# Kernel tuning notes

Hardware: AMD Instinct MI355X
Metric: run time of the kernel (lower is better)

## Reference

```python
import jax, jax.numpy as jnp
import numpy as np

N_FFT = 256
HOP = 64            # fft_stride
WIN_LEN = 1024      # window_length (samples)
STRIDE = 256        # MPF window stride (samples)
FS = 2000.0
BANDS = [(0.0, 25.0), (25.0, 50.0), (50.0, 100.0), (100.0, 200.0), (200.0, 400.0), (400.0, 1000.0)]


def setup_inputs() -> dict:
    key = jax.random.key(0)
    x = jax.random.normal(key, (8, 32, 16000), dtype=jnp.float32)
    return {"inputs": x}


def _mpf_forward(inputs):
    # --- channelwise STFT (center=False, onesided, hann periodic=False) ---
    window = jnp.asarray(np.hanning(N_FFT), dtype=inputs.dtype)  # matches torch.hann_window(periodic=False)
    wnorm = jnp.linalg.norm(window)
    B, C, T = inputs.shape
    n_frames = 1 + (T - N_FFT) // HOP
    fidx = np.arange(n_frames)[:, None] * HOP + np.arange(N_FFT)[None, :]
    frames = inputs[..., fidx]                       # (B, C, n_frames, n_fft)
    spec = jnp.fft.rfft(frames * window, axis=-1) / wnorm  # (B, C, n_frames, F)
    spec = jnp.swapaxes(spec, -1, -2)                # (B, C, F, n_frames)

    # --- sliding window over STFT frames ---
    size = WIN_LEN // HOP   # 16
    step = STRIDE // HOP    # 4
    n_win = (n_frames - size) // step + 1
    widx = np.arange(n_win)[:, None] * step + np.arange(size)[None, :]
    win = spec[..., widx]                            # (B, C, F, n_win, size)
    x = jnp.transpose(win, (0, 3, 2, 1, 4))          # (B, n_win, F, C, size)

    # --- cross-spectral density: X X^H / size, then |.|^2 ---
    csd = jnp.einsum('btfcw,btfdw->btfcd', x, jnp.conj(x)) / size
    csd = csd.real ** 2 + csd.imag ** 2              # (B, n_win, F, C, C) real

    # --- average FFT bins into frequency bands ---
    freqs = np.fft.rfftfreq(N_FFT, d=1.0 / FS)
    masks_np = np.stack([(freqs > lo) & (freqs <= hi) for lo, hi in BANDS]).astype(np.float32)
    masks = jnp.asarray(masks_np, dtype=csd.dtype)   # (n_bands, F)
    banded = jnp.einsum('btfcd,kf->btkcd', csd, masks) / masks.sum(axis=1)[None, None, :, None, None]

    # --- SPD matrix log via eigh, eigvals floored at 100*eps ---
    eigvals, eigvecs = jnp.linalg.eigh(banded)
    floor = 100.0 * jnp.finfo(banded.dtype).eps
    log_vals = jnp.log(jnp.maximum(eigvals, floor))
    out = jnp.einsum('...ij,...j,...kj->...ik', eigvecs, log_vals, eigvecs)

    # (batch, time, bands, c1, c2) -> (batch, bands, c1, c2, time)
    return jnp.transpose(out, (0, 2, 3, 4, 1))


def reference(inputs) -> jnp.ndarray:
    return _mpf_forward(inputs)
```

## Files before the change

### kernel.cpp

```cpp
#include <hip/hip_runtime.h>
#include <cstddef>

#define NFRM 247
#define NBIN 128
#define NC   32
#define NWIN 58
#define NMAT (8 * NWIN * 6)

__global__ __launch_bounds__(128) void k_stft(const float* __restrict__ x,
                                              float2* __restrict__ spec) {
  const int gid = blockIdx.x;
  const int fr  = gid % NFRM;
  const int bc  = gid / NFRM;
  const int tid = threadIdx.x;

  __shared__ float  xw[256];
  __shared__ float2 Y[256];

  const float* xp = x + ((size_t)bc * 16000 + (size_t)fr * 64);

  #pragma unroll
  for (int k = 0; k < 2; ++k) {
    const int t = tid + k * 128;
    const float wv = 0.5f - 0.5f * __cosf((float)t * 0.024639942f);
    xw[t] = xp[t] * wv * 0.10226200f;
  }
  __syncthreads();

  #pragma unroll
  for (int k = 0; k < 2; ++k) {
    const int e = tid + k * 128;
    const int f0 = e >> 4, t0 = e & 15;
    float sA, cA;
    __sincosf((float)f0 * 0.39269908f, &sA, &cA);
    float wr = 1.f, wi = 0.f, re = 0.f, im = 0.f;
    #pragma unroll
    for (int t1 = 0; t1 < 16; ++t1) {
      const float v = xw[(t1 << 4) + t0];
      re = fmaf(v, wr, re);
      im = fmaf(v, wi, im);
      const float nwr = fmaf(wi, sA, wr * cA);
      const float nwi = fmaf(-wr, sA, wi * cA);
      wr = nwr; wi = nwi;
    }
    Y[e] = make_float2(re, im);
  }
  __syncthreads();

  const int f = tid + 1;
  const int f0 = f & 15;
  float sB, cB;
  __sincosf((float)f * 0.024543693f, &sB, &cB);
  float wr = 1.f, wi = 0.f, re = 0.f, im = 0.f;
  #pragma unroll
  for (int t0 = 0; t0 < 16; ++t0) {
    const float2 yv = Y[(f0 << 4) + t0];
    re += yv.x * wr - yv.y * wi;
    im += yv.x * wi + yv.y * wr;
    const float nwr = fmaf(wi, sB, wr * cB);
    const float nwi = fmaf(-wr, sB, wi * cB);
    wr = nwr; wi = nwi;
  }
  const int b = bc >> 5, c = bc & 31;
  spec[(((size_t)b * NFRM + fr) * NBIN + (f - 1)) * NC + c] = make_float2(re, im);
}

__global__ __launch_bounds__(256) void k_csd(const float2* __restrict__ spec,
                                             float* __restrict__ part, int P) {
  const int bt  = blockIdx.x;
  const int p   = blockIdx.y;
  const int b   = bt / NWIN, t = bt % NWIN;
  const int tid = threadIdx.x;
  const int wv  = tid >> 6;
  const int lane = tid & 63;
  const int i0 = (lane >> 3) * 4;
  const int j0 = (lane & 7) * 4;

  __shared__ __align__(16) char smemraw[32768];
  float2 (*rng)[2][512] = reinterpret_cast<float2 (*)[2][512]>(smemraw);
  float* red = reinterpret_cast<float*>(smemraw);

  float bacc[6][16];
  #pragma unroll
  for (int k = 0; k < 6; ++k)
    #pragma unroll
    for (int e = 0; e < 16; ++e) bacc[k][e] = 0.f;

  const float2* sb = spec + (size_t)b * NFRM * NBIN * NC;
  const int itn = 32 / P;

  #define STG_LOAD(itl, dst)                                                     \
    {                                                                            \
      const int f_ = 1 + wv + 4 * (itn * p + (itl));                             \
      const float2* fp_ = sb + (size_t)(f_ - 1) * NC;                            \
      _Pragma("unroll")                                                          \
      for (int r = 0; r < 8; ++r) {                                              \
        const int e_ = lane + r * 64;                                            \
        dst[r] = fp_[(size_t)(t * 4 + (e_ >> 5)) * (NBIN * NC) + (e_ & 31)];     \
      }                                                                          \
    }

  {
    float2 stg[8];
    STG_LOAD(0, stg)
    float2* Xs = rng[wv][0];
    #pragma unroll
    for (int r = 0; r < 8; ++r) Xs[lane + r * 64] = stg[r];
  }

  for (int itl = 0; itl < itn; ++itl) {
    float2 stg2[8];
    if (itl + 1 < itn) STG_LOAD(itl + 1, stg2)

    const int f = 1 + wv + 4 * (itn * p + itl);
    const float2* Xs = rng[wv][itl & 1];

    float accRe[16], accIm[16];
    #pragma unroll
    for (int e = 0; e < 16; ++e) { accRe[e] = 0.f; accIm[e] = 0.f; }

    #pragma unroll
    for (int s = 0; s < 16; ++s) {
      float2 xi[4], xj[4];
      #pragma unroll
      for (int a = 0; a < 4; ++a) {
        xi[a] = Xs[s * 32 + i0 + a];
        xj[a] = Xs[s * 32 + j0 + a];
      }
      #pragma unroll
      for (int a = 0; a < 4; ++a)
        #pragma unroll
        for (int d = 0; d < 4; ++d) {
          const int e = a * 4 + d;
          accRe[e] = fmaf(xi[a].x, xj[d].x, fmaf(xi[a].y, xj[d].y, accRe[e]));
          accIm[e] = fmaf(xi[a].y, xj[d].x, fmaf(-xi[a].x, xj[d].y, accIm[e]));
        }
    }

    #define ACCB(K) { _Pragma("unroll") \
      for (int e = 0; e < 16; ++e) { float rr = accRe[e], ii = accIm[e]; \
        bacc[K][e] = fmaf(rr, rr, fmaf(ii, ii, bacc[K][e])); } }
    if      (f <= 3)  ACCB(0)
    else if (f <= 6)  ACCB(1)
    else if (f <= 12) ACCB(2)
    else if (f <= 25) ACCB(3)
    else if (f <= 51) ACCB(4)
    else              ACCB(5)
    #undef ACCB

    if (itl + 1 < itn) {
      float2* Xn = rng[wv][(itl + 1) & 1];
      #pragma unroll
      for (int r = 0; r < 8; ++r) Xn[lane + r * 64] = stg2[r];
    }
  }
  #undef STG_LOAD

  __syncthreads();

  for (int w2 = 0; w2 < 4; ++w2) {
    if (wv == w2) {
      #pragma unroll
      for (int k = 0; k < 6; ++k)
        #pragma unroll
        for (int a = 0; a < 4; ++a)
          #pragma unroll
          for (int d = 0; d < 4; ++d) {
            const int idx = k * 1024 + (i0 + a) * 32 + (j0 + d);
            const float v = bacc[k][a * 4 + d];
            if (w2 == 0) red[idx] = v; else red[idx] += v;
          }
    }
    __syncthreads();
  }

  float* op = part + ((size_t)p * (8 * NWIN) + bt) * 6144;
  for (int u = tid; u < 6144; u += 256) {
    const int k = u >> 10;
    float scl;
    if      (k <= 1) scl = 1.f / 768.f;
    else if (k == 2) scl = 1.f / 1536.f;
    else if (k == 3) scl = 1.f / 3328.f;
    else if (k == 4) scl = 1.f / 6656.f;
    else             scl = 1.f / 19712.f;
    op[u] = red[u] * scl;
  }
}

__global__ __launch_bounds__(64) void k_eig(const float* __restrict__ part,
                                            float* __restrict__ eigTmp, int P) {
  const int blk  = blockIdx.x;
  const int lane = threadIdx.x;
  const int h    = lane >> 5;
  const int c    = lane & 31;

  __shared__ float sA[32][36];
  __shared__ float sSc[32];

  for (int u = lane; u < 1024; u += 64) {
    const size_t base = (size_t)blk * 1024 + u;
    float s = 0.f;
    for (int p = 0; p < P; ++p) s += part[(size_t)p * ((size_t)NMAT * 1024) + base];
    sA[u >> 5][u & 31] = s;
  }
  __syncthreads();

  float g[16];
  #pragma unroll
  for (int i = 0; i < 16; ++i) g[i] = sA[16 * h + i][c];

  float n;
  {
    float p0 = 0.f, p1 = 0.f, p2 = 0.f, p3 = 0.f;
    #pragma unroll
    for (int e = 0; e < 16; e += 4) {
      p0 = fmaf(g[e + 0], g[e + 0], p0);
      p1 = fmaf(g[e + 1], g[e + 1], p1);
      p2 = fmaf(g[e + 2], g[e + 2], p2);
      p3 = fmaf(g[e + 3], g[e + 3], p3);
    }
    const float pp = (p0 + p1) + (p2 + p3);
    const float op = __shfl_xor(pp, 32);
    n = h ? (op + pp) : (pp + op);
  }

  const float EPS2 = 1e-7f;
  #pragma unroll 1
  for (int sweep = 0; sweep < 10; ++sweep) {
    int anybad = 0;
    #pragma unroll 1
    for (int m = 1; m < 32; ++m) {
      const int pidx = (lane ^ m) << 2;
      float tmp[16];
      #pragma unroll
      for (int e = 0; e < 16; ++e)
        tmp[e] = __int_as_float(__builtin_amdgcn_ds_bpermute(pidx, __float_as_int(g[e])));
      const float np = __int_as_float(__builtin_amdgcn_ds_bpermute(pidx, __float_as_int(n)));

      float d0 = 0.f, d1 = 0.f, d2 = 0.f, d3 = 0.f;
      #pragma unroll
      for (int e = 0; e < 16; e += 4) {
        d0 = fmaf(g[e + 0], tmp[e + 0], d0);
        d1 = fmaf(g[e + 1], tmp[e + 1], d1);
        d2 = fmaf(g[e + 2], tmp[e + 2], d2);
        d3 = fmaf(g[e + 3], tmp[e + 3], d3);
      }
      const float pp = (d0 + d1) + (d2 + d3);
      const float op = __shfl_xor(pp, 32);
      const float bpq = h ? (op + pp) : (pp + op);

      const int bad = (bpq * bpq > EPS2 * n * np);
      anybad |= bad;
      if (bad) {
        const float tau = (np - n) * 0.5f * __builtin_amdgcn_rcpf(bpq);
        float tf = __builtin_amdgcn_rcpf(fabsf(tau) + __builtin_amdgcn_sqrtf(fmaf(tau, tau, 1.f)));
        if (tau < 0.f) tf = -tf;
        const float cr = __builtin_amdgcn_rsqf(fmaf(tf, tf, 1.f));
        const float sg = -tf * cr;
        n = fmaf(-tf, bpq, n);
        #pragma unroll
        for (int e = 0; e < 16; ++e) g[e] = fmaf(sg, tmp[e], cr * g[e]);
      }
    }
    if (!__any(anybad)) break;
  }

  float nx;
  {
    float p0 = 0.f, p1 = 0.f, p2 = 0.f, p3 = 0.f;
    #pragma unroll
    for (int e = 0; e < 16; e += 4) {
      p0 = fmaf(g[e + 0], g[e + 0], p0);
      p1 = fmaf(g[e + 1], g[e + 1], p1);
      p2 = fmaf(g[e + 2], g[e + 2], p2);
      p3 = fmaf(g[e + 3], g[e + 3], p3);
    }
    const float pp = (p0 + p1) + (p2 + p3);
    const float op = __shfl_xor(pp, 32);
    nx = h ? (op + pp) : (pp + op);
  }
  const float lv = 0.5f * __logf(fmaxf(nx, 1.4210855e-10f));
  const float sc = (nx > 1e-32f) ? (lv * __builtin_amdgcn_rcpf(nx)) : 0.f;

  __syncthreads();
  #pragma unroll
  for (int i = 0; i < 16; ++i) sA[c][16 * h + i] = g[i];
  if (h == 0) sSc[c] = sc;
  __syncthreads();

  float a[32];
  #pragma unroll
  for (int e = 0; e < 32; ++e) a[e] = sSc[e] * sA[e][c];

  float* ob = eigTmp + ((size_t)blk * 1024 + c * 32 + 16 * h);
  #pragma unroll
  for (int q = 0; q < 4; ++q) {
    float4 acc = make_float4(0.f, 0.f, 0.f, 0.f);
    #pragma unroll
    for (int e = 0; e < 32; ++e) {
      const float4 gv = *(const float4*)&sA[e][16 * h + 4 * q];
      acc.x = fmaf(a[e], gv.x, acc.x);
      acc.y = fmaf(a[e], gv.y, acc.y);
      acc.z = fmaf(a[e], gv.z, acc.z);
      acc.w = fmaf(a[e], gv.w, acc.w);
    }
    *(float4*)(ob + 4 * q) = acc;
  }
}

__global__ __launch_bounds__(256) void k_tr(const float* __restrict__ eigTmp,
                                            float* __restrict__ out) {
  const int bk    = blockIdx.x >> 3;
  const int chunk = blockIdx.x & 7;
  const int b = bk / 6, k = bk % 6;
  const int ij0 = chunk * 128;
  const int tid = threadIdx.x;

  __shared__ float tile[128 * 59];

  for (int u = tid; u < 128 * NWIN; u += 256) {
    const int t = u >> 7, ijl = u & 127;
    tile[ijl * 59 + t] = eigTmp[((size_t)(b * NWIN + t) * 6 + k) * 1024 + ij0 + ijl];
  }
  __syncthreads();

  float* ob = out + ((size_t)bk * 1024 + ij0) * NWIN;
  for (int u = tid; u < 128 * NWIN; u += 256) {
    ob[u] = tile[(u / NWIN) * 59 + (u % NWIN)];
  }
}

extern "C" void kernel_launch(void* const* d_in, const int* in_sizes, int n_in,
                              void* d_out, int out_size, void* d_ws, size_t ws_size,
                              hipStream_t stream) {
  const float* x = (const float*)d_in[0];
  float* outp = (float*)d_out;

  const size_t SPEC_B = (size_t)8 * NFRM * NBIN * NC * sizeof(float2);
  const size_t BAND_B = (size_t)NMAT * 1024 * sizeof(float);

  float2* spec   = (float2*)d_ws;
  float*  part   = (float*)((char*)d_ws + SPEC_B);
  float*  eigTmp = (float*)d_ws;

  int P = 1;
  if (ws_size >= SPEC_B + 2 * BAND_B) P = 2;

  k_stft<<<dim3(8 * 32 * NFRM), dim3(128), 0, stream>>>(x, spec);
  k_csd <<<dim3(8 * NWIN, P),   dim3(256), 0, stream>>>(spec, part, P);
  k_eig <<<dim3(NMAT),          dim3(64),  0, stream>>>(part, eigTmp, P);
  k_tr  <<<dim3(48 * 8),        dim3(256), 0, stream>>>(eigTmp, outp);
}
```

Before: 455.1 us.

## Split CSD frequency accumulation into two specialized phase kernels

Replaces the single CSD kernel, which split frequencies into P halves, with two templated kernels covering bins 1-48 (five bands) and 49-128 (two bands). Each kernel keeps only the band accumulators it needs, which cuts register pressure and lets the launch bounds request higher occupancy. It also reorders block indices so consecutive blocks are spread across batches. The eig kernel now reads the two partial buffers and sums only band 4, which spans both phases. In exchange there is one extra kernel launch, and the two phases do unequal amounts of work.

```diff
diff --git a/kernel.cpp b/kernel.cpp
--- a/kernel.cpp
+++ b/kernel.cpp
@@ -6,6 +6,7 @@
 #define NC   32
 #define NWIN 58
 #define NMAT (8 * NWIN * 6)
+#define NBT  (8 * NWIN)
 
 __global__ __launch_bounds__(128) void k_stft(const float* __restrict__ x,
                                               float2* __restrict__ spec) {
@@ -65,10 +66,14 @@
   spec[(((size_t)b * NFRM + fr) * NBIN + (f - 1)) * NC + c] = make_float2(re, im);
 }
 
-__global__ __launch_bounds__(256) void k_csd(const float2* __restrict__ spec,
-                                             float* __restrict__ part, int P) {
-  const int bt  = blockIdx.x;
-  const int p   = blockIdx.y;
+template<int PHASE>
+__global__ __launch_bounds__(256, PHASE == 0 ? 3 : 4)
+void k_csd(const float2* __restrict__ spec, float* __restrict__ part) {
+  constexpr int FSTART = PHASE == 0 ? 1 : 49;
+  constexpr int ITN    = PHASE == 0 ? 12 : 20;
+  constexpr int NB     = PHASE == 0 ? 5 : 2;
+
+  const int bt  = (blockIdx.x & 7) * 58 + (blockIdx.x >> 3);
   const int b   = bt / NWIN, t = bt % NWIN;
   const int tid = threadIdx.x;
   const int wv  = tid >> 6;
@@ -80,18 +85,17 @@
   float2 (*rng)[2][512] = reinterpret_cast<float2 (*)[2][512]>(smemraw);
   float* red = reinterpret_cast<float*>(smemraw);
 
-  float bacc[6][16];
-  #pragma unroll
-  for (int k = 0; k < 6; ++k)
+  float bacc[NB][16];
+  #pragma unroll
+  for (int k = 0; k < NB; ++k)
     #pragma unroll
     for (int e = 0; e < 16; ++e) bacc[k][e] = 0.f;
 
   const float2* sb = spec + (size_t)b * NFRM * NBIN * NC;
-  const int itn = 32 / P;
 
   #define STG_LOAD(itl, dst)                                                     \
     {                                                                            \
-      const int f_ = 1 + wv + 4 * (itn * p + (itl));                             \
+      const int f_ = FSTART + wv + 4 * (itl);                                    \
       const float2* fp_ = sb + (size_t)(f_ - 1) * NC;                            \
       _Pragma("unroll")                                                          \
       for (int r = 0; r < 8; ++r) {                                              \
@@ -108,11 +112,11 @@
     for (int r = 0; r < 8; ++r) Xs[lane + r * 64] = stg[r];
   }
 
-  for (int itl = 0; itl < itn; ++itl) {
+  for (int itl = 0; itl < ITN; ++itl) {
     float2 stg2[8];
-    if (itl + 1 < itn) STG_LOAD(itl + 1, stg2)
-
-    const int f = 1 + wv + 4 * (itn * p + itl);
+    if (itl + 1 < ITN) STG_LOAD(itl + 1, stg2)
+
+    const int f = FSTART + wv + 4 * itl;
     const float2* Xs = rng[wv][itl & 1];
 
     float accRe[16], accIm[16];
@@ -140,15 +144,19 @@
     #define ACCB(K) { _Pragma("unroll") \
       for (int e = 0; e < 16; ++e) { float rr = accRe[e], ii = accIm[e]; \
         bacc[K][e] = fmaf(rr, rr, fmaf(ii, ii, bacc[K][e])); } }
-    if      (f <= 3)  ACCB(0)
-    else if (f <= 6)  ACCB(1)
-    else if (f <= 12) ACCB(2)
-    else if (f <= 25) ACCB(3)
-    else if (f <= 51) ACCB(4)
-    else              ACCB(5)
+    if constexpr (PHASE == 0) {
+      if      (f <= 3)  ACCB(0)
+      else if (f <= 6)  ACCB(1)
+      else if (f <= 12) ACCB(2)
+      else if (f <= 25) ACCB(3)
+      else              ACCB(4)
+    } else {
+      if      (f <= 51) ACCB(0)
+      else              ACCB(1)
+    }
     #undef ACCB
 
-    if (itl + 1 < itn) {
+    if (itl + 1 < ITN) {
       float2* Xn = rng[wv][(itl + 1) & 1];
       #pragma unroll
       for (int r = 0; r < 8; ++r) Xn[lane + r * 64] = stg2[r];
@@ -161,7 +169,7 @@
   for (int w2 = 0; w2 < 4; ++w2) {
     if (wv == w2) {
       #pragma unroll
-      for (int k = 0; k < 6; ++k)
+      for (int k = 0; k < NB; ++k)
         #pragma unroll
         for (int a = 0; a < 4; ++a)
           #pragma unroll
@@ -174,33 +182,42 @@
     __syncthreads();
   }
 
-  float* op = part + ((size_t)p * (8 * NWIN) + bt) * 6144;
-  for (int u = tid; u < 6144; u += 256) {
+  float* op = part + (size_t)bt * (NB * 1024);
+  for (int u = tid; u < NB * 1024; u += 256) {
     const int k = u >> 10;
     float scl;
-    if      (k <= 1) scl = 1.f / 768.f;
-    else if (k == 2) scl = 1.f / 1536.f;
-    else if (k == 3) scl = 1.f / 3328.f;
-    else if (k == 4) scl = 1.f / 6656.f;
-    else             scl = 1.f / 19712.f;
+    if constexpr (PHASE == 0) {
+      if      (k <= 1) scl = 1.f / 768.f;
+      else if (k == 2) scl = 1.f / 1536.f;
+      else if (k == 3) scl = 1.f / 3328.f;
+      else             scl = 1.f / 6656.f;
+    } else {
+      scl = (k == 0) ? (1.f / 6656.f)
+                     : (1.f / 19712.f);
+    }
     op[u] = red[u] * scl;
   }
 }
 
-__global__ __launch_bounds__(64) void k_eig(const float* __restrict__ part,
-                                            float* __restrict__ eigTmp, int P) {
+__global__ __launch_bounds__(64) void k_eig(const float* __restrict__ partA,
+                                            const float* __restrict__ partB,
+                                            float* __restrict__ eigTmp) {
   const int blk  = blockIdx.x;
   const int lane = threadIdx.x;
   const int h    = lane >> 5;
   const int c    = lane & 31;
 
+  const int kq = blk % 6;
+  const int bt = blk / 6;
+
   __shared__ float sA[32][36];
   __shared__ float sSc[32];
 
   for (int u = lane; u < 1024; u += 64) {
-    const size_t base = (size_t)blk * 1024 + u;
-    float s = 0.f;
-    for (int p = 0; p < P; ++p) s += part[(size_t)p * ((size_t)NMAT * 1024) + base];
+    float s;
+    if (kq <= 3)      s = partA[(size_t)bt * 5120 + kq * 1024 + u];
+    else if (kq == 4) s = partA[(size_t)bt * 5120 + 4096 + u] + partB[(size_t)bt * 2048 + u];
+    else              s = partB[(size_t)bt * 2048 + 1024 + u];
     sA[u >> 5][u & 31] = s;
   }
   __syncthreads();
@@ -336,18 +353,17 @@
   const float* x = (const float*)d_in[0];
   float* outp = (float*)d_out;
 
-  const size_t SPEC_B = (size_t)8 * NFRM * NBIN * NC * sizeof(float2);
-  const size_t BAND_B = (size_t)NMAT * 1024 * sizeof(float);
+  const size_t SPEC_B  = (size_t)8 * NFRM * NBIN * NC * sizeof(float2);
+  const size_t PARTA_B = (size_t)NBT * 5120 * sizeof(float);
 
   float2* spec   = (float2*)d_ws;
-  float*  part   = (float*)((char*)d_ws + SPEC_B);
+  float*  partA  = (float*)((char*)d_ws + SPEC_B);
+  float*  partB  = (float*)((char*)d_ws + SPEC_B + PARTA_B);
   float*  eigTmp = (float*)d_ws;
 
-  int P = 1;
-  if (ws_size >= SPEC_B + 2 * BAND_B) P = 2;
-
-  k_stft<<<dim3(8 * 32 * NFRM), dim3(128), 0, stream>>>(x, spec);
-  k_csd <<<dim3(8 * NWIN, P),   dim3(256), 0, stream>>>(spec, part, P);
-  k_eig <<<dim3(NMAT),          dim3(64),  0, stream>>>(part, eigTmp, P);
-  k_tr  <<<dim3(48 * 8),        dim3(256), 0, stream>>>(eigTmp, outp);
-}
+  k_stft   <<<dim3(8 * 32 * NFRM), dim3(128), 0, stream>>>(x, spec);
+  k_csd<0> <<<dim3(NBT),           dim3(256), 0, stream>>>(spec, partA);
+  k_csd<1> <<<dim3(NBT),           dim3(256), 0, stream>>>(spec, partB);
+  k_eig    <<<dim3(NMAT),          dim3(64),  0, stream>>>(partA, partB, eigTmp);
+  k_tr     <<<dim3(48 * 8),        dim3(256), 0, stream>>>(eigTmp, outp);
+}
```

Measured after the change: 492.7 us. 1.08x slower.

## Assign contiguous frequency ranges per wave and drop shared-memory band reduction

Applied to the files above, without the earlier changes.

Each wave now processes 16 consecutive frequency bins instead of interleaved bins, so it keeps one running band accumulator and writes a partial matrix to a per-slot buffer whenever it crosses a band boundary. This removes the 6x16 register accumulator array, the serialized four-step shared-memory reduction with syncthreads, and the 24KB reduction pass. The eigen kernel then sums a variable number of slot partials per band. It also always launches the split-by-2 grid and assumes the workspace holds 13 slots of partials without checking ws_size.

```diff
diff --git a/kernel.cpp b/kernel.cpp
--- a/kernel.cpp
+++ b/kernel.cpp
@@ -6,6 +6,7 @@
 #define NC   32
 #define NWIN 58
 #define NMAT (8 * NWIN * 6)
+#define NBT  (8 * NWIN)
 
 __global__ __launch_bounds__(128) void k_stft(const float* __restrict__ x,
                                               float2* __restrict__ spec) {
@@ -66,7 +67,7 @@
 }
 
 __global__ __launch_bounds__(256) void k_csd(const float2* __restrict__ spec,
-                                             float* __restrict__ part, int P) {
+                                             float* __restrict__ part) {
   const int bt  = blockIdx.x;
   const int p   = blockIdx.y;
   const int b   = bt / NWIN, t = bt % NWIN;
@@ -76,22 +77,42 @@
   const int i0 = (lane >> 3) * 4;
   const int j0 = (lane & 7) * 4;
 
-  __shared__ __align__(16) char smemraw[32768];
-  float2 (*rng)[2][512] = reinterpret_cast<float2 (*)[2][512]>(smemraw);
-  float* red = reinterpret_cast<float*>(smemraw);
-
-  float bacc[6][16];
-  #pragma unroll
-  for (int k = 0; k < 6; ++k)
-    #pragma unroll
-    for (int e = 0; e < 16; ++e) bacc[k][e] = 0.f;
+  __shared__ __align__(16) float2 rng[4][2][512];
+
+  float bacc[16];
+  #pragma unroll
+  for (int e = 0; e < 16; ++e) bacc[e] = 0.f;
 
   const float2* sb = spec + (size_t)b * NFRM * NBIN * NC;
-  const int itn = 32 / P;
+  const int fbase = 1 + 64 * p + 16 * wv;
+  int slot = p ? (9 + wv) : (wv == 0 ? 0 : wv == 1 ? 4 : wv == 2 ? 6 : 7);
+
+  #define BANDOF(f) ((f) <= 3 ? 0 : (f) <= 6 ? 1 : (f) <= 12 ? 2 : (f) <= 25 ? 3 : (f) <= 51 ? 4 : 5)
+  int curband = BANDOF(fbase);
+
+  #define FLUSH()                                                                \
+    {                                                                            \
+      float scl_;                                                                \
+      switch (curband) {                                                         \
+        case 0: case 1: scl_ = 1.f / 768.f;   break;                             \
+        case 2:         scl_ = 1.f / 1536.f;  break;                             \
+        case 3:         scl_ = 1.f / 3328.f;  break;                             \
+        case 4:         scl_ = 1.f / 6656.f;  break;                             \
+        default:        scl_ = 1.f / 19712.f; break;                             \
+      }                                                                          \
+      float* op_ = part + ((size_t)slot * NBT + bt) * 1024;                      \
+      _Pragma("unroll")                                                          \
+      for (int a = 0; a < 4; ++a)                                                \
+        *(float4*)(op_ + (i0 + a) * 32 + j0) =                                   \
+          make_float4(bacc[a * 4 + 0] * scl_, bacc[a * 4 + 1] * scl_,            \
+                      bacc[a * 4 + 2] * scl_, bacc[a * 4 + 3] * scl_);           \
+      _Pragma("unroll")                                                          \
+      for (int e = 0; e < 16; ++e) bacc[e] = 0.f;                                \
+    }
 
   #define STG_LOAD(itl, dst)                                                     \
     {                                                                            \
-      const int f_ = 1 + wv + 4 * (itn * p + (itl));                             \
+      const int f_ = fbase + (itl);                                              \
       const float2* fp_ = sb + (size_t)(f_ - 1) * NC;                            \
       _Pragma("unroll")                                                          \
       for (int r = 0; r < 8; ++r) {                                              \
@@ -103,16 +124,22 @@
   {
     float2 stg[8];
     STG_LOAD(0, stg)
-    float2* Xs = rng[wv][0];
-    #pragma unroll
-    for (int r = 0; r < 8; ++r) Xs[lane + r * 64] = stg[r];
-  }
-
-  for (int itl = 0; itl < itn; ++itl) {
+    #pragma unroll
+    for (int r = 0; r < 8; ++r) rng[wv][0][lane + r * 64] = stg[r];
+  }
+
+  #pragma unroll 1
+  for (int itl = 0; itl < 16; ++itl) {
     float2 stg2[8];
-    if (itl + 1 < itn) STG_LOAD(itl + 1, stg2)
-
-    const int f = 1 + wv + 4 * (itn * p + itl);
+    if (itl + 1 < 16) STG_LOAD(itl + 1, stg2)
+
+    const int f = fbase + itl;
+    if (f == 4 || f == 7 || f == 13 || f == 26 || f == 52) {
+      FLUSH()
+      ++slot;
+      curband = BANDOF(f);
+    }
+
     const float2* Xs = rng[wv][itl & 1];
 
     float accRe[16], accIm[16];
@@ -137,70 +164,40 @@
         }
     }
 
-    #define ACCB(K) { _Pragma("unroll") \
-      for (int e = 0; e < 16; ++e) { float rr = accRe[e], ii = accIm[e]; \
-        bacc[K][e] = fmaf(rr, rr, fmaf(ii, ii, bacc[K][e])); } }
-    if      (f <= 3)  ACCB(0)
-    else if (f <= 6)  ACCB(1)
-    else if (f <= 12) ACCB(2)
-    else if (f <= 25) ACCB(3)
-    else if (f <= 51) ACCB(4)
-    else              ACCB(5)
-    #undef ACCB
-
-    if (itl + 1 < itn) {
-      float2* Xn = rng[wv][(itl + 1) & 1];
-      #pragma unroll
-      for (int r = 0; r < 8; ++r) Xn[lane + r * 64] = stg2[r];
-    }
-  }
+    #pragma unroll
+    for (int e = 0; e < 16; ++e)
+      bacc[e] = fmaf(accRe[e], accRe[e], fmaf(accIm[e], accIm[e], bacc[e]));
+
+    if (itl + 1 < 16) {
+      #pragma unroll
+      for (int r = 0; r < 8; ++r) rng[wv][(itl + 1) & 1][lane + r * 64] = stg2[r];
+    }
+  }
+  FLUSH()
   #undef STG_LOAD
-
-  __syncthreads();
-
-  for (int w2 = 0; w2 < 4; ++w2) {
-    if (wv == w2) {
-      #pragma unroll
-      for (int k = 0; k < 6; ++k)
-        #pragma unroll
-        for (int a = 0; a < 4; ++a)
-          #pragma unroll
-          for (int d = 0; d < 4; ++d) {
-            const int idx = k * 1024 + (i0 + a) * 32 + (j0 + d);
-            const float v = bacc[k][a * 4 + d];
-            if (w2 == 0) red[idx] = v; else red[idx] += v;
-          }
-    }
-    __syncthreads();
-  }
-
-  float* op = part + ((size_t)p * (8 * NWIN) + bt) * 6144;
-  for (int u = tid; u < 6144; u += 256) {
-    const int k = u >> 10;
-    float scl;
-    if      (k <= 1) scl = 1.f / 768.f;
-    else if (k == 2) scl = 1.f / 1536.f;
-    else if (k == 3) scl = 1.f / 3328.f;
-    else if (k == 4) scl = 1.f / 6656.f;
-    else             scl = 1.f / 19712.f;
-    op[u] = red[u] * scl;
-  }
+  #undef FLUSH
+  #undef BANDOF
 }
 
 __global__ __launch_bounds__(64) void k_eig(const float* __restrict__ part,
-                                            float* __restrict__ eigTmp, int P) {
+                                            float* __restrict__ eigTmp) {
   const int blk  = blockIdx.x;
   const int lane = threadIdx.x;
   const int h    = lane >> 5;
   const int c    = lane & 31;
 
+  const int kq = blk % 6;
+  const int bt = blk / 6;
+  const int s0  = (kq <= 2) ? kq : (kq == 3 ? 3 : kq == 4 ? 5 : 8);
+  const int cnt = (kq <= 2) ? 1  : (kq == 3 ? 2 : kq == 4 ? 3 : 5);
+
   __shared__ float sA[32][36];
   __shared__ float sSc[32];
 
   for (int u = lane; u < 1024; u += 64) {
-    const size_t base = (size_t)blk * 1024 + u;
     float s = 0.f;
-    for (int p = 0; p < P; ++p) s += part[(size_t)p * ((size_t)NMAT * 1024) + base];
+    for (int q = 0; q < cnt; ++q)
+      s += part[((size_t)(s0 + q) * NBT + bt) * 1024 + u];
     sA[u >> 5][u & 31] = s;
   }
   __syncthreads();
@@ -337,17 +334,13 @@
   float* outp = (float*)d_out;
 
   const size_t SPEC_B = (size_t)8 * NFRM * NBIN * NC * sizeof(float2);
-  const size_t BAND_B = (size_t)NMAT * 1024 * sizeof(float);
 
   float2* spec   = (float2*)d_ws;
   float*  part   = (float*)((char*)d_ws + SPEC_B);
   float*  eigTmp = (float*)d_ws;
 
-  int P = 1;
-  if (ws_size >= SPEC_B + 2 * BAND_B) P = 2;
-
   k_stft<<<dim3(8 * 32 * NFRM), dim3(128), 0, stream>>>(x, spec);
-  k_csd <<<dim3(8 * NWIN, P),   dim3(256), 0, stream>>>(spec, part, P);
-  k_eig <<<dim3(NMAT),          dim3(64),  0, stream>>>(part, eigTmp, P);
+  k_csd <<<dim3(NBT, 2),        dim3(256), 0, stream>>>(spec, part);
+  k_eig <<<dim3(NMAT),          dim3(64),  0, stream>>>(part, eigTmp);
   k_tr  <<<dim3(48 * 8),        dim3(256), 0, stream>>>(eigTmp, outp);
 }
```

Measured after the change: 437.7 us. 1.04x faster.
